# Optimization experiments

Hardware: AMD Instinct MI355X
Metric: run time of the kernel (lower is better)

Reference implementation:

```python
import jax, jax.numpy as jnp
import numpy as np

K1 = 3                      # spline kernel size per pseudo dim
SIZE = float(np.sqrt(2.0))  # pseudo_cartesian normalization size


def spline_weights(p, k):
    """Degree-1 open B-spline basis over 2D pseudo coords.
    p: [..., 2] in [0,1]. Returns basis [..., 4], weight_index [..., 4]."""
    v = jnp.clip(p, 0.0, 1.0) * (k - 1)
    lo = jnp.floor(v)
    frac = v - lo
    lo = lo.astype(jnp.int32)
    off = jnp.array([0, 1], dtype=jnp.int32)
    w0 = jnp.stack([1.0 - frac[..., 0], frac[..., 0]], axis=-1)   # [...,2]
    w1 = jnp.stack([1.0 - frac[..., 1], frac[..., 1]], axis=-1)   # [...,2]
    i0 = jnp.clip(lo[..., 0:1] + off, 0, k - 1)                    # [...,2]
    i1 = jnp.clip(lo[..., 1:2] + off, 0, k - 1)                    # [...,2]
    basis = (w0[..., :, None] * w1[..., None, :]).reshape(*p.shape[:-1], 4)
    widx = (i0[..., :, None] + k * i1[..., None, :]).reshape(*p.shape[:-1], 4)
    return basis, widx


def setup_inputs() -> dict:
    key = jax.random.key(0)
    kx, ke, kp, kq, kw, kb = jax.random.split(key, 6)
    N, C, P, E, K = 50000, 64, 16, 800000, K1 * K1
    x = jax.random.normal(kx, (N, C), dtype=jnp.float32)
    pos = jax.random.uniform(kp, (N, 2), dtype=jnp.float32)
    pose = jax.random.normal(kq, (N, P, 2), dtype=jnp.float32)
    pose = pose / (jnp.linalg.norm(pose, axis=-1, keepdims=True) + 1e-8)  # unit pose vectors
    W = jax.random.normal(kw, (P, K, C), dtype=jnp.float32) / np.sqrt(C * 4.0)
    bias = jax.random.normal(kb, (P,), dtype=jnp.float32) * 0.01
    edge_index = jax.random.randint(ke, (2, E), 0, N, dtype=jnp.int64)
    return {"x": x, "pos": pos, "pose": pose, "W": W, "bias": bias,
            "edge_index": edge_index}


def reference(x, pos, pose, W, bias, edge_index):
    N, C = x.shape
    P = pose.shape[1]
    row, col = edge_index[0], edge_index[1]
    # pseudo_cartesian: normalized relative position in [0,1]^2
    pseudo = (pos[col] - pos[row]) / (2.0 * SIZE) + 0.5              # [E,2]
    # posevec_to_rotmat on detached pose vectors
    pose_c = jax.lax.stop_gradient(pose)
    a, b = pose_c[..., 0], pose_c[..., 1]
    R = jnp.stack([jnp.stack([a, -b], -1), jnp.stack([b, a], -1)], -2)  # [N,P,2,2]
    Re = R[row]                                                      # [E,P,2,2]
    # rotate pseudo coords about (0.5, 0.5), batched over all poses
    p = jnp.einsum('epij,ej->epi', Re, pseudo - 0.5) + 0.5           # [E,P,2]
    basis, widx = spline_weights(p, K1)                              # [E,P,4]
    # SplineConv (out_channels=1, no root weight, no norm):
    # precompute per-node per-pose per-kernel-bin projections
    Z = jnp.einsum('nc,pkc->npk', x, W)                              # [N,P,K]
    pidx = jnp.arange(P)[None, :, None]
    vals = Z[col[:, None, None], pidx, widx]                         # [E,P,4]
    msg = jnp.sum(basis * vals, axis=-1)                             # [E,P]
    out = jax.ops.segment_sum(msg, row, num_segments=N)              # [N,P]
    return out + bias[None, :]
```

## Files before the change

### kernel.cpp

```cpp
#include <hip/hip_runtime.h>

#define C_DIM 64
#define P_DIM 16
#define K_DIM 9
#define ZROW 10
#define ZNODE (P_DIM * ZROW)
#define NT 10
#define INV2S 0.35355339059327373f

typedef __attribute__((ext_vector_type(8))) short short8v;
typedef __attribute__((ext_vector_type(4))) float f32x4;

__device__ __forceinline__ ushort f2bf(float f) {
    uint u = __builtin_bit_cast(uint, f);
    return (ushort)((u + 0x7FFFu + ((u >> 16) & 1u)) >> 16);
}
__device__ __forceinline__ float bf2f(ushort h) {
    return __builtin_bit_cast(float, ((uint)h) << 16);
}

#define WSTRIDE 72

__global__ __launch_bounds__(256) void z_gemm_kernel(const float* __restrict__ x,
                                                     const float* __restrict__ W,
                                                     const float* __restrict__ bias,
                                                     float* __restrict__ out,
                                                     ushort* __restrict__ Zb,
                                                     int N) {
    __shared__ ushort w_hi[160 * WSTRIDE];
    __shared__ ushort w_lo[160 * WSTRIDE];

    const int tid = threadIdx.x;
    const int block_row = blockIdx.x * 64;

    {
        const float4 b4 = ((const float4*)bias)[tid & 3];
        const int o4 = block_row * 4 + tid;
        if (o4 < N * 4) ((float4*)out)[o4] = b4;
    }

    for (int i = tid; i < 160 * (C_DIM / 2); i += 256) {
        const int s  = i >> 5;
        const int k2 = i & 31;
        const int p  = s / 10;
        const int k  = s - p * 10;
        float2 w2 = make_float2(0.0f, 0.0f);
        if (k < 9) w2 = ((const float2*)W)[(p * 9 + k) * (C_DIM / 2) + k2];
        const int o = s * WSTRIDE + k2 * 2;
        const ushort h0 = f2bf(w2.x);
        const ushort h1 = f2bf(w2.y);
        w_hi[o]     = h0;
        w_hi[o + 1] = h1;
        w_lo[o]     = f2bf(w2.x - bf2f(h0));
        w_lo[o + 1] = f2bf(w2.y - bf2f(h1));
    }
    __syncthreads();

    const int lane = tid & 63;
    const int wv   = tid >> 6;
    const int col  = lane & 15;
    const int kg   = lane >> 4;

    const int arow = block_row + wv * 16 + col;
    const float* xr = x + (size_t)(arow < N ? arow : 0) * C_DIM;
    float4 x0 = ((const float4*)xr)[kg * 2];
    float4 x1 = ((const float4*)xr)[kg * 2 + 1];
    float4 x2 = ((const float4*)xr)[8 + kg * 2];
    float4 x3 = ((const float4*)xr)[8 + kg * 2 + 1];
    if (arow >= N) {
        x0 = x1 = x2 = x3 = make_float4(0.f, 0.f, 0.f, 0.f);
    }

    short8v a_hi0, a_lo0, a_hi1, a_lo1;
    {
        const float t0[8] = {x0.x, x0.y, x0.z, x0.w, x1.x, x1.y, x1.z, x1.w};
        const float t1[8] = {x2.x, x2.y, x2.z, x2.w, x3.x, x3.y, x3.z, x3.w};
        #pragma unroll
        for (int e = 0; e < 8; ++e) {
            const ushort h = f2bf(t0[e]);
            a_hi0[e] = (short)h;
            a_lo0[e] = (short)f2bf(t0[e] - bf2f(h));
            const ushort g = f2bf(t1[e]);
            a_hi1[e] = (short)g;
            a_lo1[e] = (short)f2bf(t1[e] - bf2f(g));
        }
    }

    const int orow0 = block_row + wv * 16 + kg * 4;

    #pragma unroll
    for (int nt = 0; nt < NT; ++nt) {
        const int j = nt * 16 + col;
        const ushort* bhp = &w_hi[j * WSTRIDE + kg * 8];
        const ushort* blp = &w_lo[j * WSTRIDE + kg * 8];
        const short8v bh0 = *(const short8v*)bhp;
        const short8v bh1 = *(const short8v*)(bhp + 32);
        const short8v bl0 = *(const short8v*)blp;
        const short8v bl1 = *(const short8v*)(blp + 32);

        f32x4 acc = {0.f, 0.f, 0.f, 0.f};
        acc = __builtin_amdgcn_mfma_f32_16x16x32_bf16(a_lo0, bh0, acc, 0, 0, 0);
        acc = __builtin_amdgcn_mfma_f32_16x16x32_bf16(a_hi0, bl0, acc, 0, 0, 0);
        acc = __builtin_amdgcn_mfma_f32_16x16x32_bf16(a_lo1, bh1, acc, 0, 0, 0);
        acc = __builtin_amdgcn_mfma_f32_16x16x32_bf16(a_hi1, bl1, acc, 0, 0, 0);
        acc = __builtin_amdgcn_mfma_f32_16x16x32_bf16(a_hi0, bh0, acc, 0, 0, 0);
        acc = __builtin_amdgcn_mfma_f32_16x16x32_bf16(a_hi1, bh1, acc, 0, 0, 0);

        #pragma unroll
        for (int r = 0; r < 4; ++r) {
            const int row = orow0 + r;
            if (row < N) Zb[(size_t)row * ZNODE + j] = f2bf(acc[r]);
        }
    }
}

#define EILP 8
__global__ __launch_bounds__(256) void edge_kernel(const int* __restrict__ ei,
                                                   const float* __restrict__ pos,
                                                   const float* __restrict__ pose,
                                                   const ushort* __restrict__ Zb,
                                                   float* __restrict__ out,
                                                   int E) {
    const int p  = threadIdx.x & 15;
    const int eg = threadIdx.x >> 4;
    const int e0 = blockIdx.x * (16 * EILP) + eg;

    int  r[EILP], c[EILP];
    bool valid[EILP];
    #pragma unroll
    for (int it = 0; it < EILP; ++it) {
        int e = e0 + it * 16;
        valid[it] = (e < E);
        int ec = valid[it] ? e : 0;
        r[it] = ei[ec];
        c[it] = ei[E + ec];
    }

    float d0[EILP], d1[EILP];
    #pragma unroll
    for (int it = 0; it < EILP; ++it) {
        const float2 pc = ((const float2*)pos)[c[it]];
        const float2 pr = ((const float2*)pos)[r[it]];
        d0[it] = (pc.x - pr.x) * INV2S;
        d1[it] = (pc.y - pr.y) * INV2S;
    }

    float a_[EILP], b_[EILP];
    #pragma unroll
    for (int it = 0; it < EILP; ++it) {
        const float2 ab = ((const float2*)pose)[(size_t)r[it] * P_DIM + p];
        a_[it] = ab.x;
        b_[it] = ab.y;
    }

    uint q0[EILP], q1[EILP], q2[EILP], q3[EILP], q4[EILP];
    #pragma unroll
    for (int it = 0; it < EILP; ++it) {
        const uint* Zp = (const uint*)(Zb + (size_t)c[it] * ZNODE) + p * (ZROW / 2);
        q0[it] = Zp[0];
        q1[it] = Zp[1];
        q2[it] = Zp[2];
        q3[it] = Zp[3];
        q4[it] = Zp[4];
    }

    #pragma unroll
    for (int it = 0; it < EILP; ++it) {
        const float p0 = fmaf(a_[it], d0[it], fmaf(-b_[it], d1[it], 0.5f));
        const float p1 = fmaf(b_[it], d0[it], fmaf( a_[it], d1[it], 0.5f));

        const float v0 = fminf(fmaxf(p0, 0.0f), 1.0f) * 2.0f;
        const float v1 = fminf(fmaxf(p1, 0.0f), 1.0f) * 2.0f;
        const bool b0 = (v0 >= 1.0f);
        const bool b1 = (v1 >= 1.0f);
        const float f0 = v0 - (b0 ? 1.0f : 0.0f);
        const float f1 = v1 - (b1 ? 1.0f : 0.0f);

        const uint A0 = q0[it], A1 = q1[it], A2 = q2[it], A3 = q3[it], A4 = q4[it];
        const uint W0 = b1 ? ((A1 >> 16) | (A2 << 16)) : A0;
        const uint W1 = b1 ? ((A2 >> 16) | (A3 << 16)) : A1;
        const uint W2 = b1 ? ((A3 >> 16) | (A4 << 16)) : A2;
        const uint s = b0 ? 16u : 0u;
        const float z00 = bf2f((ushort)(W0 >> s));
        const float z10 = bf2f((ushort)(b0 ? (W1 & 0xffffu) : (W0 >> 16)));
        const float z01 = bf2f((ushort)(b0 ? (W2 & 0xffffu) : (W1 >> 16)));
        const float z11 = bf2f((ushort)(W2 >> s));

        const float w00 = (1.0f - f0) * (1.0f - f1);
        const float w01 = (1.0f - f0) * f1;
        const float w10 = f0 * (1.0f - f1);
        const float w11 = f0 * f1;

        float m = w00 * z00;
        m = fmaf(w01, z01, m);
        m = fmaf(w10, z10, m);
        m = fmaf(w11, z11, m);

        if (valid[it]) atomicAdd(&out[(size_t)r[it] * P_DIM + p], m);
    }
}

extern "C" void kernel_launch(void* const* d_in, const int* in_sizes, int n_in,
                              void* d_out, int out_size, void* d_ws, size_t ws_size,
                              hipStream_t stream) {
    const float* x    = (const float*)d_in[0];
    const float* pos  = (const float*)d_in[1];
    const float* pose = (const float*)d_in[2];
    const float* W    = (const float*)d_in[3];
    const float* bias = (const float*)d_in[4];
    const int*   ei   = (const int*)d_in[5];

    const int N = in_sizes[0] / C_DIM;
    const int E = in_sizes[5] / 2;

    float* out = (float*)d_out;
    ushort* Zb = (ushort*)d_ws;

    z_gemm_kernel<<<(N + 63) / 64, 256, 0, stream>>>(x, W, bias, out, Zb, N);

    const int eblocks = (E + 16 * EILP - 1) / (16 * EILP);
    edge_kernel<<<eblocks, 256, 0, stream>>>(ei, pos, pose, Zb, out, E);
}
```

Measured before the change: 153.6 us.

## Pack pose vectors to bf16, vectorize Z loads, split edge launch in two

```diff
diff --git a/kernel.cpp b/kernel.cpp
--- a/kernel.cpp
+++ b/kernel.cpp
@@ -10,6 +10,7 @@
 
 typedef __attribute__((ext_vector_type(8))) short short8v;
 typedef __attribute__((ext_vector_type(4))) float f32x4;
+typedef uint uint4a __attribute__((ext_vector_type(4), aligned(4)));
 
 __device__ __forceinline__ ushort f2bf(float f) {
     uint u = __builtin_bit_cast(uint, f);
@@ -24,8 +25,10 @@
 __global__ __launch_bounds__(256) void z_gemm_kernel(const float* __restrict__ x,
                                                      const float* __restrict__ W,
                                                      const float* __restrict__ bias,
+                                                     const float* __restrict__ pose,
                                                      float* __restrict__ out,
                                                      ushort* __restrict__ Zb,
+                                                     uint* __restrict__ pose_bf,
                                                      int N) {
     __shared__ ushort w_hi[160 * WSTRIDE];
     __shared__ ushort w_lo[160 * WSTRIDE];
@@ -37,6 +40,17 @@
         const float4 b4 = ((const float4*)bias)[tid & 3];
         const int o4 = block_row * 4 + tid;
         if (o4 < N * 4) ((float4*)out)[o4] = b4;
+    }
+
+    if (pose_bf != nullptr) {
+        for (int i = tid; i < 64 * P_DIM; i += 256) {
+            const int r = block_row + (i >> 4);
+            if (r < N) {
+                const float2 ab = ((const float2*)pose)[(size_t)r * P_DIM + (i & 15)];
+                pose_bf[(size_t)r * P_DIM + (i & 15)] =
+                    (uint)f2bf(ab.x) | ((uint)f2bf(ab.y) << 16);
+            }
+        }
     }
 
     for (int i = tid; i < 160 * (C_DIM / 2); i += 256) {
@@ -115,22 +129,24 @@
 }
 
 #define EILP 8
+template <bool USEBF>
 __global__ __launch_bounds__(256) void edge_kernel(const int* __restrict__ ei,
                                                    const float* __restrict__ pos,
                                                    const float* __restrict__ pose,
+                                                   const uint* __restrict__ pose_bf,
                                                    const ushort* __restrict__ Zb,
                                                    float* __restrict__ out,
-                                                   int E) {
+                                                   int E, int ebase, int eend) {
     const int p  = threadIdx.x & 15;
     const int eg = threadIdx.x >> 4;
-    const int e0 = blockIdx.x * (16 * EILP) + eg;
+    const int e0 = ebase + blockIdx.x * (16 * EILP) + eg;
 
     int  r[EILP], c[EILP];
     bool valid[EILP];
     #pragma unroll
     for (int it = 0; it < EILP; ++it) {
         int e = e0 + it * 16;
-        valid[it] = (e < E);
+        valid[it] = (e < eend);
         int ec = valid[it] ? e : 0;
         r[it] = ei[ec];
         c[it] = ei[E + ec];
@@ -148,19 +164,23 @@
     float a_[EILP], b_[EILP];
     #pragma unroll
     for (int it = 0; it < EILP; ++it) {
-        const float2 ab = ((const float2*)pose)[(size_t)r[it] * P_DIM + p];
-        a_[it] = ab.x;
-        b_[it] = ab.y;
-    }
-
-    uint q0[EILP], q1[EILP], q2[EILP], q3[EILP], q4[EILP];
+        if (USEBF) {
+            const uint ab = pose_bf[(size_t)r[it] * P_DIM + p];
+            a_[it] = bf2f((ushort)(ab & 0xffffu));
+            b_[it] = bf2f((ushort)(ab >> 16));
+        } else {
+            const float2 ab = ((const float2*)pose)[(size_t)r[it] * P_DIM + p];
+            a_[it] = ab.x;
+            b_[it] = ab.y;
+        }
+    }
+
+    uint4a qv[EILP];
+    uint   q4[EILP];
     #pragma unroll
     for (int it = 0; it < EILP; ++it) {
         const uint* Zp = (const uint*)(Zb + (size_t)c[it] * ZNODE) + p * (ZROW / 2);
-        q0[it] = Zp[0];
-        q1[it] = Zp[1];
-        q2[it] = Zp[2];
-        q3[it] = Zp[3];
+        qv[it] = *(const uint4a*)Zp;
         q4[it] = Zp[4];
     }
 
@@ -176,7 +196,8 @@
         const float f0 = v0 - (b0 ? 1.0f : 0.0f);
         const float f1 = v1 - (b1 ? 1.0f : 0.0f);
 
-        const uint A0 = q0[it], A1 = q1[it], A2 = q2[it], A3 = q3[it], A4 = q4[it];
+        const uint A0 = qv[it][0], A1 = qv[it][1], A2 = qv[it][2],
+                   A3 = qv[it][3], A4 = q4[it];
         const uint W0 = b1 ? ((A1 >> 16) | (A2 << 16)) : A0;
         const uint W1 = b1 ? ((A2 >> 16) | (A3 << 16)) : A1;
         const uint W2 = b1 ? ((A3 >> 16) | (A4 << 16)) : A2;
@@ -216,8 +237,21 @@
     float* out = (float*)d_out;
     ushort* Zb = (ushort*)d_ws;
 
-    z_gemm_kernel<<<(N + 63) / 64, 256, 0, stream>>>(x, W, bias, out, Zb, N);
-
-    const int eblocks = (E + 16 * EILP - 1) / (16 * EILP);
-    edge_kernel<<<eblocks, 256, 0, stream>>>(ei, pos, pose, Zb, out, E);
-}
+    const size_t zb_bytes   = (size_t)N * ZNODE * sizeof(ushort);
+    const size_t pose_bytes = (size_t)N * P_DIM * sizeof(uint);
+    uint* pose_bf = (ws_size >= zb_bytes + pose_bytes)
+                        ? (uint*)((char*)d_ws + zb_bytes) : nullptr;
+
+    z_gemm_kernel<<<(N + 63) / 64, 256, 0, stream>>>(x, W, bias, pose, out, Zb, pose_bf, N);
+
+    const int Eh  = E / 2;
+    const int eb1 = (Eh + 16 * EILP - 1) / (16 * EILP);
+    const int eb2 = ((E - Eh) + 16 * EILP - 1) / (16 * EILP);
+    if (pose_bf != nullptr) {
+        edge_kernel<true><<<eb1, 256, 0, stream>>>(ei, pos, pose, pose_bf, Zb, out, E, 0, Eh);
+        edge_kernel<true><<<eb2, 256, 0, stream>>>(ei, pos, pose, pose_bf, Zb, out, E, Eh, E);
+    } else {
+        edge_kernel<false><<<eb1, 256, 0, stream>>>(ei, pos, pose, pose_bf, Zb, out, E, 0, Eh);
+        edge_kernel<false><<<eb2, 256, 0, stream>>>(ei, pos, pose, pose_bf, Zb, out, E, Eh, E);
+    }
+}
```

Result: slower. 158.5 us (+3.2%).
